# Performance work log

Measured on AMD Instinct MI355X. Metric: run time of the kernel, lower is better.

## Reference

```python
import jax, jax.numpy as jnp
import numpy as np

NEG_SLOPE = 0.2

def gat_layer(x, src, dst, W, al, ar, b):
    # x: (N, F_in); W: (F_in, H*D); al/ar: (H, D); b: (H, D)
    N = x.shape[0]
    H, D = al.shape
    feat = (x @ W).reshape(N, H, D)                      # (N,H,D)
    el = jnp.sum(feat * al, axis=-1)                     # (N,H) src-side scores
    er = jnp.sum(feat * ar, axis=-1)                     # (N,H) dst-side scores
    e = jax.nn.leaky_relu(el[src] + er[dst], NEG_SLOPE)  # (E,H)
    # edge softmax over incoming edges of each dst node (numerically stable)
    m = jax.ops.segment_max(e, dst, num_segments=N)      # (N,H)
    m = jnp.where(jnp.isfinite(m), m, 0.0)               # guard isolated nodes
    ex = jnp.exp(e - m[dst])                             # (E,H)
    denom = jax.ops.segment_sum(ex, dst, num_segments=N) # (N,H)
    alpha = ex / jnp.maximum(denom[dst], 1e-30)          # (E,H)
    msg = alpha[:, :, None] * feat[src]                  # (E,H,D) gather + weight
    out = jax.ops.segment_sum(msg, dst, num_segments=N)  # (N,H,D) scatter-add
    return out + b[None]                                 # bias per head


def setup_inputs() -> dict:
    key = jax.random.key(0)
    ks = jax.random.split(key, 12)
    N, E, F_in, Dh = 100000, 1600000, 128, 64
    H1 = 2
    inp = {}
    inp['in_feat'] = jax.random.normal(ks[0], (N, F_in), dtype=jnp.float32)
    inp['src'] = jax.random.randint(ks[1], (E,), 0, N, dtype=jnp.int32)
    inp['dst'] = jax.random.randint(ks[2], (E,), 0, N, dtype=jnp.int32)
    s1 = 1.0 / np.sqrt(F_in)
    inp['W1'] = jax.random.normal(ks[3], (F_in, H1 * Dh), dtype=jnp.float32) * s1
    inp['al1'] = jax.random.normal(ks[4], (H1, Dh), dtype=jnp.float32) * 0.1
    inp['ar1'] = jax.random.normal(ks[5], (H1, Dh), dtype=jnp.float32) * 0.1
    inp['b1'] = jnp.zeros((H1, Dh), dtype=jnp.float32)
    s2 = 1.0 / np.sqrt(Dh)
    inp['W2'] = jax.random.normal(ks[6], (Dh, 1 * 2), dtype=jnp.float32) * s2
    inp['al2'] = jax.random.normal(ks[7], (1, 2), dtype=jnp.float32) * 0.1
    inp['ar2'] = jax.random.normal(ks[8], (1, 2), dtype=jnp.float32) * 0.1
    inp['b2'] = jnp.zeros((1, 2), dtype=jnp.float32)
    return inp


def reference(in_feat, src, dst, W1, al1, ar1, b1, W2, al2, ar2, b2):
    num_heads = al1.shape[0]
    h = gat_layer(in_feat, src, dst, W1, al1, ar1, b1)  # (N,2,64)
    h = jnp.sum(h, axis=1) / num_heads                  # head mean
    h = jax.nn.relu(h)
    out = gat_layer(h, src, dst, W2, al2, ar2, b2)      # (N,1,2)
    return out
```

## Files before the change

kernel.cpp:

```cpp
#include <hip/hip_runtime.h>
#include <hip/hip_bf16.h>
#include <hip/hip_fp16.h>

#define LEAKY 0.2f
#define NBMAX 1024
#define CCH   4096
#define SCAP2 3456

typedef _Float16 half8 __attribute__((ext_vector_type(8)));
typedef float f32x4 __attribute__((ext_vector_type(4)));

__device__ __forceinline__ float wave_sum64(float v) {
    #pragma unroll
    for (int m = 32; m > 0; m >>= 1) v += __shfl_xor(v, m, 64);
    return v;
}

__launch_bounds__(256)
__global__ void w1cvt_kernel(const float* __restrict__ W, __half* __restrict__ Wt) {
    int i = blockIdx.x * 256 + threadIdx.x;
    int n = i >> 7, k = i & 127;
    Wt[i] = __float2half(W[k * 128 + n]);
}

__launch_bounds__(256)
__global__ void gemm1_kernel(const float* __restrict__ X, const __half* __restrict__ Wt,
                             const float* __restrict__ al1, const float* __restrict__ ar1,
                             unsigned char* __restrict__ feat8, __half* __restrict__ sch,
                             float* __restrict__ el1, float* __restrict__ er1, int N) {
    __shared__ __half Al[64 * 136];
    __shared__ __half Wl[128 * 136];
    const int tid = threadIdx.x;
    const int r0 = blockIdx.x * 64;
    {
        int n = tid >> 1, h0 = (tid & 1) * 64;
        const __half* gsrc = Wt + n * 128 + h0;
        __half* ldst = Wl + n * 136 + h0;
        #pragma unroll
        for (int i = 0; i < 8; i++)
            *(uint4*)(ldst + i * 8) = *(const uint4*)(gsrc + i * 8);
    }
    {
        int r = tid >> 2, c0 = (tid & 3) * 32;
        int rr = r0 + r;
        const float* gsrc = X + (size_t)rr * 128 + c0;
        __half* ldst = Al + r * 136 + c0;
        if (rr < N) {
            #pragma unroll
            for (int i = 0; i < 8; i++) {
                float4 v = *(const float4*)(gsrc + i * 4);
                __half2 a = __floats2half2_rn(v.x, v.y);
                __half2 b = __floats2half2_rn(v.z, v.w);
                uint2 pk; pk.x = *(unsigned*)&a; pk.y = *(unsigned*)&b;
                *(uint2*)(ldst + i * 4) = pk;
            }
        } else {
            uint2 z; z.x = 0; z.y = 0;
            #pragma unroll
            for (int i = 0; i < 8; i++) *(uint2*)(ldst + i * 4) = z;
        }
    }
    __syncthreads();
    const int wv = tid >> 6, lane = tid & 63;
    const int lm = lane & 15, lq = lane >> 4;
    f32x4 acc[8];
    #pragma unroll
    for (int t = 0; t < 8; t++) acc[t] = (f32x4){0.f, 0.f, 0.f, 0.f};
    const __half* arow = Al + (wv * 16 + lm) * 136 + lq * 8;
    const __half* brow = Wl + lm * 136 + lq * 8;
    #pragma unroll
    for (int ks = 0; ks < 4; ks++) {
        half8 af = *(const half8*)(arow + ks * 32);
        #pragma unroll
        for (int nt = 0; nt < 8; nt++) {
            half8 bf = *(const half8*)(brow + nt * 16 * 136 + ks * 32);
            acc[nt] = __builtin_amdgcn_mfma_f32_16x16x32_f16(af, bf, acc[nt], 0, 0, 0);
        }
    }
    __syncthreads();
    __half* Cl = Al;
    #pragma unroll
    for (int nt = 0; nt < 8; nt++) {
        #pragma unroll
        for (int r = 0; r < 4; r++) {
            int m = wv * 16 + lq * 4 + r;
            Cl[m * 136 + nt * 16 + lm] = __float2half(acc[nt][r]);
        }
    }
    __syncthreads();
    {
        int r = tid >> 2, c0 = (tid & 3) * 32;
        int rr = r0 + r;
        float pel = 0.f, per = 0.f;
        const __half* crow = Cl + r * 136 + c0;
        if (rr < N) {
            float am = 0.f;
            #pragma unroll
            for (int c = 0; c < 32; c++) {
                float fv = __half2float(crow[c]);
                pel += fv * al1[c0 + c];
                per += fv * ar1[c0 + c];
                am = fmaxf(am, fabsf(fv));
            }
            am = fmaxf(am, __shfl_xor(am, 1, 64));
            am = fmaxf(am, __shfl_xor(am, 2, 64));
            float s = __half2float(__float2half_rn(fmaxf(am, 1e-8f) * (1.f / 127.5f)));
            float is = 1.f / s;
            unsigned pk8[8];
            #pragma unroll
            for (int i = 0; i < 8; i++) {
                unsigned w = 0;
                #pragma unroll
                for (int k = 0; k < 4; k++) {
                    float fv = __half2float(crow[i * 4 + k]);
                    int q = (int)rintf(fv * is + 127.5f);
                    q = q < 0 ? 0 : (q > 255 ? 255 : q);
                    w |= (unsigned)q << (8 * k);
                }
                pk8[i] = w;
            }
            *(uint4*)(feat8 + (size_t)rr * 128 + c0) = *(const uint4*)&pk8[0];
            *(uint4*)(feat8 + (size_t)rr * 128 + c0 + 16) = *(const uint4*)&pk8[4];
            if ((tid & 3) == 0) sch[rr] = __float2half_rn(s);
        }
        pel += __shfl_xor(pel, 1, 64);
        per += __shfl_xor(per, 1, 64);
        if ((tid & 1) == 0 && rr < N) {
            int h = (tid >> 1) & 1;
            el1[rr * 2 + h] = pel;
            er1[rr * 2 + h] = per;
        }
    }
}

__launch_bounds__(256)
__global__ void bhist_kernel(const int* __restrict__ dst, int* __restrict__ bcount,
                             int E, int NB) {
    __shared__ int hls[NBMAX];
    for (int i = threadIdx.x; i < NB; i += 256) hls[i] = 0;
    __syncthreads();
    int stride = gridDim.x * 256;
    for (int e = blockIdx.x * 256 + threadIdx.x; e < E; e += stride)
        atomicAdd(&hls[dst[e] >> 7], 1);
    __syncthreads();
    for (int i = threadIdx.x; i < NB; i += 256) {
        int c = hls[i];
        if (c) atomicAdd(&bcount[i], c);
    }
}

__launch_bounds__(1024)
__global__ void bscan_kernel(const int* __restrict__ bcount, int* __restrict__ bstart,
                             int* __restrict__ bcursor, int NB) {
    __shared__ int sd[NBMAX];
    int t = threadIdx.x;
    int v = (t < NB) ? bcount[t] : 0;
    sd[t] = v;
    __syncthreads();
    for (int o = 1; o < NBMAX; o <<= 1) {
        int x = (t >= o) ? sd[t - o] : 0;
        __syncthreads();
        sd[t] += x;
        __syncthreads();
    }
    if (t < NB) { int ex = sd[t] - v; bstart[t] = ex; bcursor[t] = ex; }
}

__launch_bounds__(256)
__global__ void bscatter_kernel(const int* __restrict__ src, const int* __restrict__ dst,
                                const float* __restrict__ el1, const float* __restrict__ er1,
                                int* __restrict__ bcursor, uint2* __restrict__ erec,
                                int E, int NB) {
    __shared__ int hls[NBMAX];
    for (int i = threadIdx.x; i < NB; i += 256) hls[i] = 0;
    __syncthreads();
    const int b0 = blockIdx.x * CCH;
    uint2 ureg[16];
    int breg[16];
    #pragma unroll
    for (int k = 0; k < 16; k++) {
        int e = b0 + k * 256 + threadIdx.x;
        if (e < E) {
            int s = src[e], d = dst[e];
            int bk = d >> 7;
            breg[k] = bk;
            float2 lv = *((const float2*)el1 + s);
            float2 rv = *((const float2*)er1 + d);
            float e0 = lv.x + rv.x; e0 = (e0 > 0.f) ? e0 : LEAKY * e0;
            float e1 = lv.y + rv.y; e1 = (e1 > 0.f) ? e1 : LEAKY * e1;
            __half2 w = __floats2half2_rn(__expf(e0), __expf(e1));
            ureg[k].x = ((unsigned)s << 7) | (unsigned)(d & 127);
            ureg[k].y = *(unsigned*)&w;
            atomicAdd(&hls[bk], 1);
        } else breg[k] = -1;
    }
    __syncthreads();
    for (int b = threadIdx.x; b < NB; b += 256) {
        int c = hls[b];
        if (c) hls[b] = atomicAdd(&bcursor[b], c);
    }
    __syncthreads();
    #pragma unroll
    for (int k = 0; k < 16; k++) {
        if (breg[k] >= 0) {
            int p = atomicAdd(&hls[breg[k]], 1);
            erec[p] = ureg[k];
        }
    }
}

__launch_bounds__(256)
__global__ void bsort_kernel(const uint2* __restrict__ erec,
                             const int* __restrict__ bstart, const int* __restrict__ bcount,
                             uint2* __restrict__ erec2,
                             int* __restrict__ rowstart, int* __restrict__ plen,
                             int* __restrict__ tlen,
                             int N, int NB) {
    __shared__ uint2 sorted[SCAP2];
    __shared__ int cnt[128], prs[129], curs[128];
    const int tid = threadIdx.x;
    const int b = blockIdx.x;
    const int node0 = b << 7;
    const int nd = min(128, N - node0);
    const int ebase = bstart[b];
    int ecnt = bcount[b];
    if (ecnt > SCAP2 - 896) ecnt = SCAP2 - 896;
    const int pbase = ebase + 896 * b;
    if (tid < 128) cnt[tid] = 0;
    __syncthreads();
    for (int j = tid; j < ecnt; j += 256)
        atomicAdd(&cnt[erec[ebase + j].x & 127], 1);
    __syncthreads();
    int pv = 0;
    if (tid < 128) { pv = (cnt[tid] + 7) & ~7; curs[tid] = pv; }
    __syncthreads();
    for (int o = 1; o < 128; o <<= 1) {
        int x = 0;
        if (tid < 128 && tid >= o) x = curs[tid - o];
        __syncthreads();
        if (tid < 128) curs[tid] += x;
        __syncthreads();
    }
    if (tid < 128) prs[tid + 1] = curs[tid];
    if (tid == 0) prs[0] = 0;
    __syncthreads();
    if (tid < 128) curs[tid] = prs[tid + 1] - pv;
    __syncthreads();
    const int pecnt = prs[128];
    for (int j = tid; j < pecnt; j += 256) { sorted[j].x = 0; sorted[j].y = 0; }
    __syncthreads();
    for (int j = tid; j < ecnt; j += 256) {
        uint2 r = erec[ebase + j];
        int p = atomicAdd(&curs[r.x & 127], 1);
        uint2 o2;
        o2.x = (r.x >> 7) << 8;
        o2.y = r.y;
        sorted[p] = o2;
    }
    __syncthreads();
    for (int j = tid; j < pecnt; j += 256) erec2[(size_t)pbase + j] = sorted[j];
    if (tid < nd) {
        rowstart[node0 + tid] = pbase + prs[tid];
        plen[node0 + tid] = prs[tid + 1] - prs[tid];
        tlen[node0 + tid] = cnt[tid];
    }
}

__device__ __forceinline__ void acc_edge8(uint2 r, unsigned v, unsigned short sh, unsigned hsh,
                                          float& a0, float& a1, float& a2, float& a3,
                                          float& den, float& csum) {
    unsigned ws = (r.y >> hsh) & 0xffffu;
    float w = __half2float(__ushort_as_half((unsigned short)ws));
    den += w;
    float s = __half2float(__ushort_as_half(sh));
    float a = w * s;
    csum += a;
    float q0 = (float)(v & 0xffu);
    float q1 = (float)((v >> 8) & 0xffu);
    float q2 = (float)((v >> 16) & 0xffu);
    float q3 = (float)(v >> 24);
    a0 += a * q0;
    a1 += a * q1;
    a2 += a * q2;
    a3 += a * q3;
}

__launch_bounds__(256)
__global__ void agg1_kernel(const char* __restrict__ fh, const __half* __restrict__ sch,
                            const uint2* __restrict__ erec2,
                            const float* __restrict__ b1, const float* __restrict__ W2,
                            const float* __restrict__ ar2,
                            const int* __restrict__ rowstart, const int* __restrict__ plen,
                            float* __restrict__ feat2, float* __restrict__ er2, int N) {
    int wid = (blockIdx.x * blockDim.x + threadIdx.x) >> 6;
    int lane = threadIdx.x & 63;
    if (wid >= N) return;
    const int len   = __builtin_amdgcn_readfirstlane(plen[wid]);
    const int rbase = __builtin_amdgcn_readfirstlane(rowstart[wid]);
    const uint2* __restrict__ rp = erec2 + rbase;
    const int l5 = lane & 31;
    const int sub = lane >> 5;
    const unsigned hsh = (l5 < 16) ? 0u : 16u;
    const unsigned lofs = (unsigned)l5 * 4u;
    float acc0 = 0.f, acc1 = 0.f, acc2 = 0.f, acc3 = 0.f, den = 0.f, csum = 0.f;

#define LDR(R, g) do { const uint2* _p = rp + ((g) * 8 + sub);                     \
        R[0] = _p[0]; R[1] = _p[2]; R[2] = _p[4]; R[3] = _p[6]; } while (0)
#define GTH(V, S, R) do {                                                          \
        V[0] = *(const unsigned*)(fh + ((R[0].x >> 1) + lofs));                    \
        V[1] = *(const unsigned*)(fh + ((R[1].x >> 1) + lofs));                    \
        V[2] = *(const unsigned*)(fh + ((R[2].x >> 1) + lofs));                    \
        V[3] = *(const unsigned*)(fh + ((R[3].x >> 1) + lofs));                    \
        S[0] = *(const unsigned short*)(sch + (R[0].x >> 8));                      \
        S[1] = *(const unsigned short*)(sch + (R[1].x >> 8));                      \
        S[2] = *(const unsigned short*)(sch + (R[2].x >> 8));                      \
        S[3] = *(const unsigned short*)(sch + (R[3].x >> 8)); } while (0)
#define ACC(R, V, S) do {                                                          \
        acc_edge8(R[0], V[0], S[0], hsh, acc0, acc1, acc2, acc3, den, csum);       \
        acc_edge8(R[1], V[1], S[1], hsh, acc0, acc1, acc2, acc3, den, csum);       \
        acc_edge8(R[2], V[2], S[2], hsh, acc0, acc1, acc2, acc3, den, csum);       \
        acc_edge8(R[3], V[3], S[3], hsh, acc0, acc1, acc2, acc3, den, csum); } while (0)

    const int n8 = len >> 3;
    if (n8 > 0) {
        uint2 ra[4], rb[4];
        unsigned va[4], vb[4];
        unsigned short sa[4], sb[4];
        LDR(ra, 0);
        if (n8 > 1) LDR(rb, 1);
        GTH(va, sa, ra);
        int g = 0;
        while (g + 1 < n8) {
            GTH(vb, sb, rb);
            ACC(ra, va, sa);
            if (g + 2 < n8) LDR(ra, g + 2);
            g++;
            if (g + 1 >= n8) { ACC(rb, vb, sb); g++; break; }
            GTH(va, sa, ra);
            ACC(rb, vb, sb);
            if (g + 2 < n8) LDR(rb, g + 2);
            g++;
        }
        if (g < n8) ACC(ra, va, sa);
    }
#undef LDR
#undef GTH
#undef ACC

    {
        float corr = 127.5f * csum;
        acc0 -= corr; acc1 -= corr; acc2 -= corr; acc3 -= corr;
    }

    acc0 += __shfl_xor(acc0, 32, 64);
    acc1 += __shfl_xor(acc1, 32, 64);
    acc2 += __shfl_xor(acc2, 32, 64);
    acc3 += __shfl_xor(acc3, 32, 64);
    den  += __shfl_xor(den,  32, 64);
    float inv = 1.f / fmaxf(den, 1e-30f);
    float4 bb = *(const float4*)(b1 + 4 * l5);
    float o0 = acc0 * inv + bb.x;
    float o1 = acc1 * inv + bb.y;
    float o2 = acc2 * inv + bb.z;
    float o3 = acc3 * inv + bb.w;
    float m0 = 0.5f * (o0 + __shfl_xor(o0, 16, 64));
    float m1 = 0.5f * (o1 + __shfl_xor(o1, 16, 64));
    float m2 = 0.5f * (o2 + __shfl_xor(o2, 16, 64));
    float m3 = 0.5f * (o3 + __shfl_xor(o3, 16, 64));
    m0 = fmaxf(m0, 0.f); m1 = fmaxf(m1, 0.f);
    m2 = fmaxf(m2, 0.f); m3 = fmaxf(m3, 0.f);
    const float* wrow = W2 + 8 * (l5 & 15);
    float4 wa = *(const float4*)wrow;
    float4 wb = *(const float4*)(wrow + 4);
    float p0 = m0 * wa.x + m1 * wa.z + m2 * wb.x + m3 * wb.z;
    float p1 = m0 * wa.y + m1 * wa.w + m2 * wb.y + m3 * wb.w;
    float c0 = 0.25f * wave_sum64(p0);
    float c1 = 0.25f * wave_sum64(p1);
    if (lane == 0) {
        float2 f2; f2.x = c0; f2.y = c1;
        *((float2*)feat2 + wid) = f2;
        er2[wid] = c0 * ar2[0] + c1 * ar2[1];
    }
}

__launch_bounds__(256)
__global__ void agg2_kernel(const float* __restrict__ feat2, const float* __restrict__ er2,
                            const float* __restrict__ al2, const float* __restrict__ b2,
                            const int* __restrict__ rowstart, const int* __restrict__ tlen,
                            const uint2* __restrict__ erec2, float* __restrict__ out, int N) {
    int node = (blockIdx.x * 256 + threadIdx.x) >> 4;
    int l4 = threadIdx.x & 15;
    if (node >= N) return;
    const int len = tlen[node];
    const uint2* rp = erec2 + rowstart[node];
    const float ern = er2[node];
    const float al20 = al2[0], al21 = al2[1];
    float den = 0.f, a0 = 0.f, a1 = 0.f;
    for (int j = l4; j < len; j += 16) {
        unsigned key = rp[j].x;
        float2 f = *((const float2*)feat2 + (key >> 8));
        float e = f.x * al20 + f.y * al21 + ern;
        e = (e > 0.f) ? e : LEAKY * e;
        float w = __expf(e);
        den += w;
        a0 += w * f.x;
        a1 += w * f.y;
    }
    #pragma unroll
    for (int m = 1; m < 16; m <<= 1) {
        den += __shfl_xor(den, m, 64);
        a0  += __shfl_xor(a0, m, 64);
        a1  += __shfl_xor(a1, m, 64);
    }
    if (l4 == 0) {
        float inv = 1.f / fmaxf(den, 1e-30f);
        float2 o;
        o.x = a0 * inv + b2[0];
        o.y = a1 * inv + b2[1];
        *((float2*)out + node) = o;
    }
}

extern "C" void kernel_launch(void* const* d_in, const int* in_sizes, int n_in,
                              void* d_out, int out_size, void* d_ws, size_t ws_size,
                              hipStream_t stream) {
    const float* in_feat = (const float*)d_in[0];
    const int*   src     = (const int*)d_in[1];
    const int*   dst     = (const int*)d_in[2];
    const float* W1      = (const float*)d_in[3];
    const float* al1     = (const float*)d_in[4];
    const float* ar1     = (const float*)d_in[5];
    const float* b1      = (const float*)d_in[6];
    const float* W2      = (const float*)d_in[7];
    const float* al2     = (const float*)d_in[8];
    const float* ar2     = (const float*)d_in[9];
    const float* b2      = (const float*)d_in[10];
    float* out = (float*)d_out;

    const int N = in_sizes[0] / 128;
    const int E = in_sizes[1];
    const int NB = (N + 127) >> 7;

    char* ws = (char*)d_ws;
    unsigned char* feat8 = (unsigned char*)ws;
    size_t off = (size_t)N * 128;
    __half* scaleh = (__half*)(ws + off); off += (size_t)N * 2;
    float* el1 = (float*)(ws + off); off += (size_t)N * 2 * 4;
    float* er1 = (float*)(ws + off); off += (size_t)N * 2 * 4;
    float* feat2 = (float*)(ws + off); off += (size_t)N * 2 * 4;
    float* er2 = (float*)(ws + off); off += (size_t)N * 4;
    int* bcount  = (int*)(ws + off); off += NBMAX * 4;
    int* bstart  = (int*)(ws + off); off += NBMAX * 4;
    int* bcursor = (int*)(ws + off); off += NBMAX * 4;
    int* rowstart = (int*)(ws + off); off += (size_t)N * 4;
    int* plen     = (int*)(ws + off); off += (size_t)N * 4;
    int* tlen     = (int*)(ws + off); off += (size_t)N * 4;
    uint2* erec  = (uint2*)(ws + off); off += (size_t)E * 8;
    uint2* erec2 = (uint2*)(ws + off); off += ((size_t)E + 896 * NB) * 8;
    __half* W1t = (__half*)(ws + off); off += 128 * 128 * 2;
    (void)ws_size; (void)n_in; (void)out_size;

    hipMemsetAsync(bcount, 0, NBMAX * 4, stream);

    w1cvt_kernel<<<64, 256, 0, stream>>>(W1, W1t);
    gemm1_kernel<<<(N + 63) / 64, 256, 0, stream>>>(in_feat, W1t, al1, ar1,
                                                    feat8, scaleh, el1, er1, N);

    const int nblkC = (E + CCH - 1) / CCH;
    bhist_kernel<<<nblkC, 256, 0, stream>>>(dst, bcount, E, NB);
    bscan_kernel<<<1, 1024, 0, stream>>>(bcount, bstart, bcursor, NB);
    bscatter_kernel<<<nblkC, 256, 0, stream>>>(src, dst, el1, er1, bcursor, erec, E, NB);
    bsort_kernel<<<NB, 256, 0, stream>>>(erec, bstart, bcount, erec2, rowstart, plen, tlen, N, NB);

    agg1_kernel<<<(N * 64 + 255) / 256, 256, 0, stream>>>(
        (const char*)feat8, scaleh, erec2, b1, W2, ar2, rowstart, plen, feat2, er2, N);

    agg2_kernel<<<(N * 16 + 255) / 256, 256, 0, stream>>>(
        feat2, er2, al2, b2, rowstart, tlen, erec2, out, N);
}
```

Baseline: 264.7 us.

## Aggregate layer-1 with 16 lanes per node and 8-byte feature gathers

agg1 now assigns 16 lanes per destination node instead of a full 64-lane wave. Each lane gathers 8 quantized feature bytes per edge (uint2) instead of 4, and the edges are no longer split across two half-waves. This packs four nodes per wave, which cuts idle lanes on low-degree nodes and drops the cross-half shuffle reduction. In exchange each lane holds more accumulator registers and does more serial work per node. The final shuffle reductions shrink to within 16 lanes.

```diff
diff --git a/kernel.cpp b/kernel.cpp
--- a/kernel.cpp
+++ b/kernel.cpp
@@ -266,23 +266,21 @@
     }
 }
 
-__device__ __forceinline__ void acc_edge8(uint2 r, unsigned v, unsigned short sh, unsigned hsh,
-                                          float& a0, float& a1, float& a2, float& a3,
-                                          float& den, float& csum) {
-    unsigned ws = (r.y >> hsh) & 0xffffu;
-    float w = __half2float(__ushort_as_half((unsigned short)ws));
+__device__ __forceinline__ void acc_edge16(uint2 r, uint2 v, unsigned short sh, unsigned hsh,
+                                           float* acc, float& den, float& csum) {
+    float w = __half2float(__ushort_as_half((unsigned short)((r.y >> hsh) & 0xffffu)));
     den += w;
     float s = __half2float(__ushort_as_half(sh));
     float a = w * s;
     csum += a;
-    float q0 = (float)(v & 0xffu);
-    float q1 = (float)((v >> 8) & 0xffu);
-    float q2 = (float)((v >> 16) & 0xffu);
-    float q3 = (float)(v >> 24);
-    a0 += a * q0;
-    a1 += a * q1;
-    a2 += a * q2;
-    a3 += a * q3;
+    acc[0] += a * (float)(v.x & 0xffu);
+    acc[1] += a * (float)((v.x >> 8) & 0xffu);
+    acc[2] += a * (float)((v.x >> 16) & 0xffu);
+    acc[3] += a * (float)(v.x >> 24);
+    acc[4] += a * (float)(v.y & 0xffu);
+    acc[5] += a * (float)((v.y >> 8) & 0xffu);
+    acc[6] += a * (float)((v.y >> 16) & 0xffu);
+    acc[7] += a * (float)(v.y >> 24);
 }
 
 __launch_bounds__(256)
@@ -292,94 +290,93 @@
                             const float* __restrict__ ar2,
                             const int* __restrict__ rowstart, const int* __restrict__ plen,
                             float* __restrict__ feat2, float* __restrict__ er2, int N) {
-    int wid = (blockIdx.x * blockDim.x + threadIdx.x) >> 6;
-    int lane = threadIdx.x & 63;
-    if (wid >= N) return;
-    const int len   = __builtin_amdgcn_readfirstlane(plen[wid]);
-    const int rbase = __builtin_amdgcn_readfirstlane(rowstart[wid]);
-    const uint2* __restrict__ rp = erec2 + rbase;
-    const int l5 = lane & 31;
-    const int sub = lane >> 5;
-    const unsigned hsh = (l5 < 16) ? 0u : 16u;
-    const unsigned lofs = (unsigned)l5 * 4u;
-    float acc0 = 0.f, acc1 = 0.f, acc2 = 0.f, acc3 = 0.f, den = 0.f, csum = 0.f;
-
-#define LDR(R, g) do { const uint2* _p = rp + ((g) * 8 + sub);                     \
-        R[0] = _p[0]; R[1] = _p[2]; R[2] = _p[4]; R[3] = _p[6]; } while (0)
+    int node = (blockIdx.x * 256 + threadIdx.x) >> 4;
+    int l4 = threadIdx.x & 15;
+    if (node >= N) return;
+    const int len = plen[node];
+    const uint2* __restrict__ rp = erec2 + rowstart[node];
+    const unsigned hsh = (l4 < 8) ? 0u : 16u;
+    const unsigned lofs = (unsigned)l4 * 8u;
+    float acc[8];
+    #pragma unroll
+    for (int k = 0; k < 8; k++) acc[k] = 0.f;
+    float den = 0.f, csum = 0.f;
+
+#define LDR(R, g) do { const uint2* _p = rp + (g) * 4;                             \
+        R[0] = _p[0]; R[1] = _p[1]; R[2] = _p[2]; R[3] = _p[3]; } while (0)
 #define GTH(V, S, R) do {                                                          \
-        V[0] = *(const unsigned*)(fh + ((R[0].x >> 1) + lofs));                    \
-        V[1] = *(const unsigned*)(fh + ((R[1].x >> 1) + lofs));                    \
-        V[2] = *(const unsigned*)(fh + ((R[2].x >> 1) + lofs));                    \
-        V[3] = *(const unsigned*)(fh + ((R[3].x >> 1) + lofs));                    \
+        V[0] = *(const uint2*)(fh + ((R[0].x >> 1) + lofs));                       \
+        V[1] = *(const uint2*)(fh + ((R[1].x >> 1) + lofs));                       \
+        V[2] = *(const uint2*)(fh + ((R[2].x >> 1) + lofs));                       \
+        V[3] = *(const uint2*)(fh + ((R[3].x >> 1) + lofs));                       \
         S[0] = *(const unsigned short*)(sch + (R[0].x >> 8));                      \
         S[1] = *(const unsigned short*)(sch + (R[1].x >> 8));                      \
         S[2] = *(const unsigned short*)(sch + (R[2].x >> 8));                      \
         S[3] = *(const unsigned short*)(sch + (R[3].x >> 8)); } while (0)
 #define ACC(R, V, S) do {                                                          \
-        acc_edge8(R[0], V[0], S[0], hsh, acc0, acc1, acc2, acc3, den, csum);       \
-        acc_edge8(R[1], V[1], S[1], hsh, acc0, acc1, acc2, acc3, den, csum);       \
-        acc_edge8(R[2], V[2], S[2], hsh, acc0, acc1, acc2, acc3, den, csum);       \
-        acc_edge8(R[3], V[3], S[3], hsh, acc0, acc1, acc2, acc3, den, csum); } while (0)
-
-    const int n8 = len >> 3;
-    if (n8 > 0) {
-        uint2 ra[4], rb[4];
-        unsigned va[4], vb[4];
+        acc_edge16(R[0], V[0], S[0], hsh, acc, den, csum);                         \
+        acc_edge16(R[1], V[1], S[1], hsh, acc, den, csum);                         \
+        acc_edge16(R[2], V[2], S[2], hsh, acc, den, csum);                         \
+        acc_edge16(R[3], V[3], S[3], hsh, acc, den, csum); } while (0)
+
+    const int n4 = len >> 2;
+    if (n4 > 0) {
+        uint2 ra[4], rb[4], va[4], vb[4];
         unsigned short sa[4], sb[4];
         LDR(ra, 0);
-        if (n8 > 1) LDR(rb, 1);
+        if (n4 > 1) LDR(rb, 1);
         GTH(va, sa, ra);
         int g = 0;
-        while (g + 1 < n8) {
+        while (g + 1 < n4) {
             GTH(vb, sb, rb);
             ACC(ra, va, sa);
-            if (g + 2 < n8) LDR(ra, g + 2);
+            if (g + 2 < n4) LDR(ra, g + 2);
             g++;
-            if (g + 1 >= n8) { ACC(rb, vb, sb); g++; break; }
+            if (g + 1 >= n4) { ACC(rb, vb, sb); g++; break; }
             GTH(va, sa, ra);
             ACC(rb, vb, sb);
-            if (g + 2 < n8) LDR(rb, g + 2);
+            if (g + 2 < n4) LDR(rb, g + 2);
             g++;
         }
-        if (g < n8) ACC(ra, va, sa);
+        if (g < n4) ACC(ra, va, sa);
     }
 #undef LDR
 #undef GTH
 #undef ACC
 
-    {
-        float corr = 127.5f * csum;
-        acc0 -= corr; acc1 -= corr; acc2 -= corr; acc3 -= corr;
-    }
-
-    acc0 += __shfl_xor(acc0, 32, 64);
-    acc1 += __shfl_xor(acc1, 32, 64);
-    acc2 += __shfl_xor(acc2, 32, 64);
-    acc3 += __shfl_xor(acc3, 32, 64);
-    den  += __shfl_xor(den,  32, 64);
-    float inv = 1.f / fmaxf(den, 1e-30f);
-    float4 bb = *(const float4*)(b1 + 4 * l5);
-    float o0 = acc0 * inv + bb.x;
-    float o1 = acc1 * inv + bb.y;
-    float o2 = acc2 * inv + bb.z;
-    float o3 = acc3 * inv + bb.w;
-    float m0 = 0.5f * (o0 + __shfl_xor(o0, 16, 64));
-    float m1 = 0.5f * (o1 + __shfl_xor(o1, 16, 64));
-    float m2 = 0.5f * (o2 + __shfl_xor(o2, 16, 64));
-    float m3 = 0.5f * (o3 + __shfl_xor(o3, 16, 64));
-    m0 = fmaxf(m0, 0.f); m1 = fmaxf(m1, 0.f);
-    m2 = fmaxf(m2, 0.f); m3 = fmaxf(m3, 0.f);
-    const float* wrow = W2 + 8 * (l5 & 15);
-    float4 wa = *(const float4*)wrow;
-    float4 wb = *(const float4*)(wrow + 4);
-    float p0 = m0 * wa.x + m1 * wa.z + m2 * wb.x + m3 * wb.z;
-    float p1 = m0 * wa.y + m1 * wa.w + m2 * wb.y + m3 * wb.w;
-    float c0 = 0.25f * wave_sum64(p0);
-    float c1 = 0.25f * wave_sum64(p1);
-    if (lane == 0) {
-        float2 f2; f2.x = c0; f2.y = c1;
-        *((float2*)feat2 + wid) = f2;
-        er2[wid] = c0 * ar2[0] + c1 * ar2[1];
+    const float corr = 127.5f * csum;
+    const float inv = 1.f / fmaxf(den, 1e-30f);
+    const float* browp = b1 + l4 * 8;
+    float4 bb0 = *(const float4*)browp;
+    float4 bb1 = *(const float4*)(browp + 4);
+    float o[8];
+    o[0] = (acc[0] - corr) * inv + bb0.x;
+    o[1] = (acc[1] - corr) * inv + bb0.y;
+    o[2] = (acc[2] - corr) * inv + bb0.z;
+    o[3] = (acc[3] - corr) * inv + bb0.w;
+    o[4] = (acc[4] - corr) * inv + bb1.x;
+    o[5] = (acc[5] - corr) * inv + bb1.y;
+    o[6] = (acc[6] - corr) * inv + bb1.z;
+    o[7] = (acc[7] - corr) * inv + bb1.w;
+    float m[8];
+    #pragma unroll
+    for (int k = 0; k < 8; k++) {
+        float t = o[k] + __shfl_xor(o[k], 8, 64);
+        m[k] = fmaxf(0.5f * t, 0.f);
+    }
+    const float* wrow = W2 + (l4 & 7) * 16;
+    float p0 = 0.f, p1 = 0.f;
+    #pragma unroll
+    for (int k = 0; k < 8; k++) {
+        p0 += m[k] * wrow[k * 2 + 0];
+        p1 += m[k] * wrow[k * 2 + 1];
+    }
+    p0 += __shfl_xor(p0, 4, 64); p0 += __shfl_xor(p0, 2, 64); p0 += __shfl_xor(p0, 1, 64);
+    p1 += __shfl_xor(p1, 4, 64); p1 += __shfl_xor(p1, 2, 64); p1 += __shfl_xor(p1, 1, 64);
+    if (l4 == 0) {
+        float2 f2; f2.x = p0; f2.y = p1;
+        *((float2*)feat2 + node) = f2;
+        er2[node] = p0 * ar2[0] + p1 * ar2[1];
     }
 }
 
@@ -472,7 +469,7 @@
     bscatter_kernel<<<nblkC, 256, 0, stream>>>(src, dst, el1, er1, bcursor, erec, E, NB);
     bsort_kernel<<<NB, 256, 0, stream>>>(erec, bstart, bcount, erec2, rowstart, plen, tlen, N, NB);
 
-    agg1_kernel<<<(N * 64 + 255) / 256, 256, 0, stream>>>(
+    agg1_kernel<<<(N * 16 + 255) / 256, 256, 0, stream>>>(
         (const char*)feat8, scaleh, erec2, b1, W2, ar2, rowstart, plen, feat2, er2, N);
 
     agg2_kernel<<<(N * 16 + 255) / 256, 256, 0, stream>>>(
```

After: 251.8 us. 4.9% less time.
